# Kernel tuning notes

Hardware: AMD Instinct MI355X
Metric: run time of the kernel (lower is better)

## Reference

```python
import jax, jax.numpy as jnp
import numpy as np

RES = 64

TRI_TABLE = jnp.array([
    [-1,-1,-1,-1,-1,-1],[1,0,2,-1,-1,-1],[4,0,3,-1,-1,-1],[1,4,2,1,3,4],
    [3,1,5,-1,-1,-1],[2,3,0,2,5,3],[1,4,0,1,5,4],[4,2,5,-1,-1,-1],
    [4,5,2,-1,-1,-1],[4,1,0,4,5,1],[3,2,0,3,5,2],[1,3,5,-1,-1,-1],
    [4,1,2,4,3,1],[3,0,4,-1,-1,-1],[2,0,1,-1,-1,-1],[-1,-1,-1,-1,-1,-1]], dtype=jnp.int32)
NUM_TRI = jnp.array([0,1,1,2,1,2,2,1,1,2,2,1,2,1,1,0], dtype=jnp.int32)
BASE_EDGES = jnp.array([0,1,0,2,0,3,1,2,1,3,2,3], dtype=jnp.int32)


def _make_tet_grid(res):
    # Kuhn 6-tet decomposition of each cube of a (res+1)^3 grid.
    n = res + 1
    ii, jj, kk = np.meshgrid(np.arange(n), np.arange(n), np.arange(n), indexing='ij')
    verts = (np.stack([ii, jj, kk], -1).reshape(-1, 3).astype(np.float32)) / res
    def vid(i, j, k):
        return (i * n + j) * n + k
    i, j, k = np.meshgrid(np.arange(res), np.arange(res), np.arange(res), indexing='ij')
    i, j, k = i.ravel(), j.ravel(), k.ravel()
    c = [vid(i + (b & 1), j + ((b >> 1) & 1), k + ((b >> 2) & 1)) for b in range(8)]
    kuhn = [(0,1,3,7),(0,3,2,7),(0,2,6,7),(0,6,4,7),(0,4,5,7),(0,5,1,7)]
    tets = np.stack([np.stack([c[a], c[b], c[d], c[e]], -1) for (a, b, d, e) in kuhn], 1)
    return verts, tets.reshape(-1, 4).astype(np.int64)


def setup_inputs() -> dict:
    key = jax.random.key(0)
    verts, tets = _make_tet_grid(RES)
    level = jax.random.normal(key, (verts.shape[0], 1), dtype=jnp.float32)
    return {"level": level, "pos": jnp.asarray(verts), "tet": jnp.asarray(tets), "threshold": 0}


def reference(level, pos, tet, threshold):
    sdf = level - threshold                    # [N,1]
    occ = sdf[:, 0] > 0                        # [N]
    occ_fx4 = occ[tet]                         # [F,4]
    occ_sum = occ_fx4.sum(-1)
    valid = (occ_sum > 0) & (occ_sum < 4)
    vt = tet[valid]                            # [Fv,4]
    occ_valid = occ_fx4[valid]                 # [Fv,4]

    edges = jnp.sort(vt[:, BASE_EDGES].reshape(-1, 2), axis=1)   # [Fv*6,2]
    unique_edges, idx_map = jnp.unique(edges, axis=0, return_inverse=True)
    idx_map = idx_map.reshape(-1)
    mask_edges = occ[unique_edges].sum(-1) == 1                  # crossing edges
    mapping = jnp.where(mask_edges, jnp.cumsum(mask_edges) - 1, -1)
    idx_map = mapping[idx_map].reshape(-1, 6)                    # [Fv,6]
    interp_v = unique_edges[mask_edges]                          # [M,2]

    p = pos[interp_v]                                            # [M,2,3]
    s = sdf[interp_v][..., 0] * jnp.array([1.0, -1.0], dtype=sdf.dtype)  # [M,2]
    w = s[:, ::-1] / s.sum(1, keepdims=True)                     # flip / denom
    verts_out = (p * w[..., None]).sum(1)                        # [M,3]

    v_id = 2 ** jnp.arange(4, dtype=jnp.int32)
    tetindex = (occ_valid.astype(jnp.int32) * v_id).sum(-1)      # [Fv]
    num_tri = NUM_TRI[tetindex]
    m1, m2 = num_tri == 1, num_tri == 2
    f1 = jnp.take_along_axis(idx_map[m1], TRI_TABLE[tetindex[m1]][:, :3], axis=1).reshape(-1, 3)
    f2 = jnp.take_along_axis(idx_map[m2], TRI_TABLE[tetindex[m2]][:, :6], axis=1).reshape(-1, 3)
    faces = jnp.concatenate([f1, f2], axis=0)
    return verts_out, faces
```

## Files before the change

kernel.cpp:

```cpp
#include <hip/hip_runtime.h>


#define RESX 64
#define NV   65
#define NV2  4225
#define NVERT 274625
#define NCUBE 262144
#define BLOCK 256
#define NG64 4292
#define CG64 4096
#define NBLK1 1073
#define CBLK 1024
#define FOLD 49
#define WINW 80
#define STAGE 9216
#define M21 0x1fffffu
#define NTRI_PACK 0x16696994u

__constant__ int c_tri[16][6] = {
    {-1,-1,-1,-1,-1,-1},{1,0,2,-1,-1,-1},{4,0,3,-1,-1,-1},{1,4,2,1,3,4},
    {3,1,5,-1,-1,-1},{2,3,0,2,5,3},{1,4,0,1,5,4},{4,2,5,-1,-1,-1},
    {4,5,2,-1,-1,-1},{4,1,0,4,5,1},{3,2,0,3,5,2},{1,3,5,-1,-1,-1},
    {4,1,2,4,3,1},{3,0,4,-1,-1,-1},{2,0,1,-1,-1,-1},{-1,-1,-1,-1,-1,-1}};
__constant__ int c_kuhn[6][4] = {{0,1,3,7},{0,3,2,7},{0,2,6,7},{0,6,4,7},{0,4,5,7},{0,5,1,7}};
__constant__ int c_off8[8] = {0,4225,65,4290,1,4226,66,4291};
__constant__ int c_loc[6][6] = {
    {0,0,0,1,1,3},{0,0,0,2,3,2},{0,0,0,2,2,6},
    {0,0,0,4,6,4},{0,0,0,4,4,5},{0,0,0,1,5,1}};
__constant__ int c_dir[6][6] = {
    {3,5,6,1,2,0},{5,1,6,3,0,4},{1,2,6,0,4,3},
    {2,0,6,1,3,5},{0,4,6,3,5,1},{4,3,6,0,1,2}};

typedef unsigned long long u64;

__device__ __forceinline__ unsigned block_scan_excl(unsigned val, unsigned* lds,
                                                    unsigned& block_total) {
    int tid = threadIdx.x, lane = tid & 63, w = tid >> 6;
    unsigned x = val;
#pragma unroll
    for (int off = 1; off < 64; off <<= 1) {
        unsigned y = (unsigned)__shfl_up((int)x, off, 64);
        if (lane >= off) x += y;
    }
    if (lane == 63) lds[w] = x;
    __syncthreads();
    if (tid == 0) {
        unsigned s = 0;
#pragma unroll
        for (int i = 0; i < 4; i++) { unsigned t = lds[i]; lds[i + 4] = s; s += t; }
        lds[8] = s;
    }
    __syncthreads();
    block_total = lds[8];
    return x - val + lds[4 + w];
}

__global__ void __launch_bounds__(256)
pass1(const float* __restrict__ level, const float* __restrict__ thrp,
      unsigned char* __restrict__ flagsArr, unsigned short* __restrict__ locEx,
      u64* __restrict__ bsAll) {
    int tid = threadIdx.x, lane = tid & 63, w = tid >> 6;
    int g = blockIdx.x * 4 + w;
    float thr = thrp[0];
    int v = g * 64 + lane;

    unsigned fl = 0;
    if (g <= 4222) {
        float a0 = level[v]        - thr;
        float a1 = level[v + 1]    - thr;
        float a2 = level[v + 65]   - thr;
        float a3 = level[v + 66]   - thr;
        float a4 = level[v + 4225] - thr;
        float a5 = level[v + 4226] - thr;
        float a6 = level[v + 4290] - thr;
        float a7 = level[v + 4291] - thr;
        int i = v / NV2; int r = v - i * NV2; int j = r / NV; int k = r - j * NV;
        bool okx = i < RESX, oky = j < RESX, okz = k < RESX;
        bool s0 = a0 > 0.f;
        fl = s0 ? 0x80u : 0u;
        if (okz               && ((a1 > 0.f) != s0)) fl |= 1u;
        if (oky               && ((a2 > 0.f) != s0)) fl |= 2u;
        if (oky && okz        && ((a3 > 0.f) != s0)) fl |= 4u;
        if (okx               && ((a4 > 0.f) != s0)) fl |= 8u;
        if (okx && okz        && ((a5 > 0.f) != s0)) fl |= 16u;
        if (okx && oky        && ((a6 > 0.f) != s0)) fl |= 32u;
        if (okx && oky && okz && ((a7 > 0.f) != s0)) fl |= 64u;
    } else if (v < NVERT) {
        int i = v / NV2; int r = v - i * NV2; int j = r / NV; int k = r - j * NV;
        bool okx = i < RESX, oky = j < RESX, okz = k < RESX;
        float a0 = level[v] - thr;
        bool s0 = a0 > 0.f;
        fl = s0 ? 0x80u : 0u;
        if (okz               && (((level[v + 1]    - thr) > 0.f) != s0)) fl |= 1u;
        if (oky               && (((level[v + 65]   - thr) > 0.f) != s0)) fl |= 2u;
        if (oky && okz        && (((level[v + 66]   - thr) > 0.f) != s0)) fl |= 4u;
        if (okx               && (((level[v + 4225] - thr) > 0.f) != s0)) fl |= 8u;
        if (okx && okz        && (((level[v + 4226] - thr) > 0.f) != s0)) fl |= 16u;
        if (okx && oky        && (((level[v + 4290] - thr) > 0.f) != s0)) fl |= 32u;
        if (okx && oky && okz && (((level[v + 4291] - thr) > 0.f) != s0)) fl |= 64u;
    }
    unsigned cnt = __popc(fl & 0x7fu);
    unsigned x = cnt;
#pragma unroll
    for (int off = 1; off < 64; off <<= 1) {
        unsigned y = (unsigned)__shfl_up((int)x, off, 64);
        if (lane >= off) x += y;
    }
    unsigned wex = x - cnt;
    unsigned totE = (unsigned)__shfl((int)x, 63, 64);
    if (v < NVERT) {
        flagsArr[v] = (unsigned char)fl;
        locEx[v] = (unsigned short)wex;
    }

    unsigned c1 = 0, c2 = 0;
    if (g < CG64) {
        int c = g * 64 + lane;
        int ci = c >> 12, cj = (c >> 6) & 63, ck = c & 63;
        int base = (ci * NV + cj) * NV + ck;
        float q0 = level[base]        - thr;
        float q4 = level[base + 1]    - thr;
        float q2 = level[base + 65]   - thr;
        float q6 = level[base + 66]   - thr;
        float q1 = level[base + 4225] - thr;
        float q5 = level[base + 4226] - thr;
        float q3 = level[base + 4290] - thr;
        float q7 = level[base + 4291] - thr;
        unsigned occ8 = (q0 > 0.f ?   1u : 0u) | (q1 > 0.f ?   2u : 0u)
                      | (q2 > 0.f ?   4u : 0u) | (q3 > 0.f ?   8u : 0u)
                      | (q4 > 0.f ?  16u : 0u) | (q5 > 0.f ?  32u : 0u)
                      | (q6 > 0.f ?  64u : 0u) | (q7 > 0.f ? 128u : 0u);
#pragma unroll
        for (int t = 0; t < 6; t++) {
            int cfg = ((occ8 >> c_kuhn[t][0]) & 1) | (((occ8 >> c_kuhn[t][1]) & 1) << 1)
                    | (((occ8 >> c_kuhn[t][2]) & 1) << 2) | (((occ8 >> c_kuhn[t][3]) & 1) << 3);
            unsigned nt = (NTRI_PACK >> (cfg << 1)) & 3u;
            c1 += (nt == 1);
            c2 += (nt == 2);
        }
        unsigned pk = c1 | (c2 << 16);
#pragma unroll
        for (int off = 32; off; off >>= 1) pk += (unsigned)__shfl_xor((int)pk, off, 64);
        c1 = pk & 0xffffu; c2 = pk >> 16;
    }
    if (lane == 0)
        bsAll[g] = (u64)totE | ((u64)c1 << 16) | ((u64)c2 << 32);
}

__global__ void __launch_bounds__(1024)
scanK(const u64* __restrict__ bsAll, uint4* __restrict__ pre) {
    __shared__ u64 lws[16];
    int tid = threadIdx.x, lane = tid & 63, w = tid >> 6;
    int b0 = tid * 5;
    u64 vl[5]; u64 s = 0;
#pragma unroll
    for (int e = 0; e < 5; e++) {
        int idx = b0 + e;
        u64 a = (idx < NG64) ? bsAll[idx] : 0ull;
        u64 p = (a & 0xffffull) | (((a >> 16) & 0xffffull) << 21)
              | (((a >> 32) & 0xffffull) << 42);
        vl[e] = p; s += p;
    }
    u64 x = s;
#pragma unroll
    for (int off = 1; off < 64; off <<= 1) {
        u64 y = __shfl_up(x, off, 64);
        if (lane >= off) x += y;
    }
    if (lane == 63) lws[w] = x;
    __syncthreads();
    if (tid == 0) {
        u64 acc = 0;
#pragma unroll
        for (int i = 0; i < 16; i++) { u64 t = lws[i]; lws[i] = acc; acc += t; }
    }
    __syncthreads();
    u64 run = x - s + lws[w];
#pragma unroll
    for (int e = 0; e < 5; e++) {
        int idx = b0 + e;
        if (idx <= NG64)
            pre[idx] = make_uint4((unsigned)(run & M21), (unsigned)((run >> 21) & M21),
                                  (unsigned)(run >> 42), 0u);
        run += vl[e];
    }
}

__device__ __forceinline__ void emit_verts_stage(
        int gidv, unsigned slotBase, const float* __restrict__ level, float thr,
        const unsigned char* __restrict__ flagsArr,
        const unsigned short* __restrict__ locEx, float* stage) {
    float lv[8];
    int gsafe = (gidv < NVERT) ? gidv : 0;
#pragma unroll
    for (int b = 0; b < 8; b++) {
        int a = gsafe + c_off8[b];
        lv[b] = level[a < NVERT ? a : 0] - thr;
    }
    if (gidv < NVERT) {
        unsigned fl = flagsArr[gidv];
        if (fl & 0x7fu) {
            int i = gidv / NV2; int r = gidv - i * NV2; int j = r / NV; int k = r - j * NV;
            float v0 = lv[0];
            unsigned slot = slotBase + locEx[gidv];
            const float inv = 1.f / 64.f;
            const int d2b[7] = {4, 2, 6, 1, 5, 3, 7};
            float fi = (float)i, fj = (float)j, fk = (float)k;
#pragma unroll
            for (int d = 0; d < 7; d++) {
                if (fl & (1u << d)) {
                    const int b = d2b[d];
                    float s1 = lv[b];
                    float w1 = v0 * __builtin_amdgcn_rcpf(v0 - s1);
                    float* o = &stage[3u * slot];
                    o[0] = (fi + (float)(b & 1) * w1) * inv;
                    o[1] = (fj + (float)((b >> 1) & 1) * w1) * inv;
                    o[2] = (fk + (float)((b >> 2) & 1) * w1) * inv;
                    slot++;
                }
            }
        }
    }
}

__global__ void __launch_bounds__(256)
pass2(const float* __restrict__ level, const float* __restrict__ thrp,
      const unsigned char* __restrict__ flagsArr,
      const unsigned short* __restrict__ locEx,
      const uint4* __restrict__ pre, float* __restrict__ out) {
    __shared__ unsigned lds[9];
    __shared__ unsigned pEw[WINW];
    __shared__ float stage[STAGE];
    int tid = threadIdx.x;
    int bid = blockIdx.x;
    int gid = bid * BLOCK + tid;
    float thr = thrp[0];
    bool hasB = (bid < FOLD);

    uint4 pA = pre[4 * bid];
    uint4 pN = pre[4 * bid + 4];
    uint4 pt = pre[NG64];
    unsigned pE = pA.x, totE_blk = pN.x - pA.x;
    unsigned p1b = pA.y, p2b = pA.z;
    unsigned M = pt.x, C1 = pt.y;

    int ci = bid >> 4, cj0 = (bid & 15) * 4;
    int vmin = (ci * NV + cj0) * NV;
    int wb = vmin >> 6;
    if (tid < WINW) {
        int t = wb + tid;
        pEw[tid] = (t <= NG64) ? pre[t].x : M;
    }

    unsigned slotBase = pre[gid >> 6].x - pE;
    emit_verts_stage(gid, slotBase, level, thr, flagsArr, locEx, stage);
    __syncthreads();
    {
        float* dst = out + 3u * pE;
        unsigned n = totE_blk * 3u;
        for (unsigned idx = tid; idx < n; idx += BLOCK)
            __builtin_nontemporal_store(stage[idx], &dst[idx]);
    }
    if (hasB) {
        int gb0 = CG64 + 4 * bid;
        unsigned pEB = pre[gb0].x;
        unsigned totB = pre[gb0 + 4].x - pEB;
        int gidB = NCUBE + bid * BLOCK + tid;
        __syncthreads();
        unsigned sbB = pre[gidB >> 6].x - pEB;
        emit_verts_stage(gidB, sbB, level, thr, flagsArr, locEx, stage);
        __syncthreads();
        float* dst = out + 3u * pEB;
        unsigned n = totB * 3u;
        for (unsigned idx = tid; idx < n; idx += BLOCK)
            __builtin_nontemporal_store(stage[idx], &dst[idx]);
    }
    __syncthreads();

    int cci = gid >> 12, ccj = (gid >> 6) & 63, cck = gid & 63;
    int base = (cci * NV + ccj) * NV + cck;
    u64 f8 = 0ull;
#pragma unroll
    for (int b = 0; b < 8; b++)
        f8 |= (u64)flagsArr[base + c_off8[b]] << (8 * b);
    unsigned occ8 = 0;
#pragma unroll
    for (int b = 0; b < 8; b++) occ8 |= (unsigned)((f8 >> (8 * b + 7)) & 1ull) << b;
    int cfgs[6];
    unsigned c1 = 0, c2 = 0;
#pragma unroll
    for (int t = 0; t < 6; t++) {
        int cfg = ((occ8 >> c_kuhn[t][0]) & 1) | (((occ8 >> c_kuhn[t][1]) & 1) << 1)
                | (((occ8 >> c_kuhn[t][2]) & 1) << 2) | (((occ8 >> c_kuhn[t][3]) & 1) << 3);
        cfgs[t] = cfg;
        unsigned nt = (NTRI_PACK >> (cfg << 1)) & 3u;
        c1 += (nt == 1); c2 += (nt == 2);
    }
    unsigned tot2;
    unsigned ex2 = block_scan_excl(c1 | (c2 << 16), lds, tot2);
    unsigned f1 = tot2 & 0xffffu;
    unsigned f2 = tot2 >> 16;
    unsigned l1c = ex2 & 0xffffu;
    unsigned l2c = ex2 >> 16;
    unsigned n1 = f1 * 3u;
#pragma unroll
    for (int t = 0; t < 6; t++) {
        int cfg = cfgs[t];
        unsigned nt = (NTRI_PACK >> (cfg << 1)) & 3u;
        if (nt == 0) continue;
        auto rank = [&](int e) -> float {
            int lc = c_loc[t][e];
            int dir = c_dir[t][e];
            int lo = base + c_off8[lc];
            unsigned flb = (unsigned)((f8 >> (8 * lc)) & 0xffull);
            return (float)(pEw[(lo >> 6) - wb] + locEx[lo]
                           + __popc(flb & ((1u << dir) - 1u)));
        };
        float ra = rank(c_tri[cfg][0]);
        float rb = rank(c_tri[cfg][1]);
        float rc = rank(c_tri[cfg][2]);
        if (nt == 1) {
            unsigned bfo = 3u * l1c;
            stage[bfo] = ra; stage[bfo + 1] = rb; stage[bfo + 2] = rc;
            l1c++;
        } else {
            float rd = rank(c_tri[cfg][4]);
            unsigned bfo = n1 + 6u * l2c;
            stage[bfo]     = ra; stage[bfo + 1] = rb; stage[bfo + 2] = rc;
            stage[bfo + 3] = ra; stage[bfo + 4] = rd; stage[bfo + 5] = rb;
            l2c++;
        }
    }
    __syncthreads();
    float* of = out + 3ull * M;
    float* o1 = of + 3u * p1b;
    for (unsigned idx = tid; idx < n1; idx += BLOCK)
        __builtin_nontemporal_store(stage[idx], &o1[idx]);
    unsigned n2 = f2 * 6u;
    float* o2 = of + 3u * (C1 + 2u * p2b);
    for (unsigned idx = tid; idx < n2; idx += BLOCK)
        __builtin_nontemporal_store(stage[n1 + idx], &o2[idx]);
}

extern "C" void kernel_launch(void* const* d_in, const int* in_sizes, int n_in,
                              void* d_out, int out_size, void* d_ws, size_t ws_size,
                              hipStream_t stream) {
    const float* level = (const float*)d_in[0];
    const float* thrp = (const float*)d_in[3];
    float* out = (float*)d_out;

    char* p = (char*)d_ws;
    unsigned char* flagsArr = (unsigned char*)p;
    p += (NVERT + 255) & ~255;
    unsigned short* locEx = (unsigned short*)p;
    p += ((sizeof(unsigned short) * NVERT) + 255) & ~255;
    u64* bsAll = (u64*)p;
    p += ((sizeof(u64) * NG64) + 255) & ~255;
    uint4* pre = (uint4*)p;

    pass1<<<NBLK1, BLOCK, 0, stream>>>(level, thrp, flagsArr, locEx, bsAll);
    scanK<<<1, 1024, 0, stream>>>(bsAll, pre);
    pass2<<<CBLK, BLOCK, 0, stream>>>(level, thrp, flagsArr, locEx, pre, out);
}
```

Baseline: 110.6 us.

## Reorganize vertex grouping to grid rows with shuffle-based neighbor reuse

```diff
diff --git a/kernel.cpp b/kernel.cpp
--- a/kernel.cpp
+++ b/kernel.cpp
@@ -7,12 +7,13 @@
 #define NVERT 274625
 #define NCUBE 262144
 #define BLOCK 256
-#define NG64 4292
-#define CG64 4096
-#define NBLK1 1073
+#define NGE 4225
+#define NGC 4096
+#define NB1I 1024
+#define NBND 129
+#define NBLK1 1057
 #define CBLK 1024
-#define FOLD 49
-#define WINW 80
+#define NFB 33
 #define STAGE 9216
 #define M21 0x1fffffu
 #define NTRI_PACK 0x16696994u
@@ -58,202 +59,267 @@
 __global__ void __launch_bounds__(256)
 pass1(const float* __restrict__ level, const float* __restrict__ thrp,
       unsigned char* __restrict__ flagsArr, unsigned short* __restrict__ locEx,
-      u64* __restrict__ bsAll) {
+      unsigned* __restrict__ bsE, unsigned* __restrict__ bsC) {
     int tid = threadIdx.x, lane = tid & 63, w = tid >> 6;
-    int g = blockIdx.x * 4 + w;
+    int bid = blockIdx.x;
     float thr = thrp[0];
-    int v = g * 64 + lane;
-
-    unsigned fl = 0;
-    if (g <= 4222) {
-        float a0 = level[v]        - thr;
-        float a1 = level[v + 1]    - thr;
-        float a2 = level[v + 65]   - thr;
-        float a3 = level[v + 66]   - thr;
-        float a4 = level[v + 4225] - thr;
-        float a5 = level[v + 4226] - thr;
-        float a6 = level[v + 4290] - thr;
-        float a7 = level[v + 4291] - thr;
-        int i = v / NV2; int r = v - i * NV2; int j = r / NV; int k = r - j * NV;
-        bool okx = i < RESX, oky = j < RESX, okz = k < RESX;
-        bool s0 = a0 > 0.f;
+    unsigned fl = 0, fl65 = 0, c1 = 0, c2 = 0;
+    int base, grp, cgrp = -1;
+
+    if (bid < NB1I) {
+        int ci = bid >> 4, cj = ((bid & 15) << 2) + w;
+        grp = ci * NV + cj;
+        base = grp * NV;
+        int v = base + lane;
+        float r0  = level[v]        - thr;
+        float rY  = level[v + 65]   - thr;
+        float rX  = level[v + 4225] - thr;
+        float rXY = level[v + 4290] - thr;
+        float t0 = 0.f, tY = 0.f, tX = 0.f, tXY = 0.f;
+        if (lane == 63) {
+            t0  = level[base + 64]   - thr;
+            tY  = level[base + 129]  - thr;
+            tX  = level[base + 4289] - thr;
+            tXY = level[base + 4354] - thr;
+        }
+        float a4 = __shfl_down(r0, 1, 64);  if (lane == 63) a4 = t0;
+        float a6 = __shfl_down(rY, 1, 64);  if (lane == 63) a6 = tY;
+        float a5 = __shfl_down(rX, 1, 64);  if (lane == 63) a5 = tX;
+        float a7 = __shfl_down(rXY, 1, 64); if (lane == 63) a7 = tXY;
+        bool s0 = r0 > 0.f;
         fl = s0 ? 0x80u : 0u;
-        if (okz               && ((a1 > 0.f) != s0)) fl |= 1u;
-        if (oky               && ((a2 > 0.f) != s0)) fl |= 2u;
-        if (oky && okz        && ((a3 > 0.f) != s0)) fl |= 4u;
-        if (okx               && ((a4 > 0.f) != s0)) fl |= 8u;
-        if (okx && okz        && ((a5 > 0.f) != s0)) fl |= 16u;
-        if (okx && oky        && ((a6 > 0.f) != s0)) fl |= 32u;
-        if (okx && oky && okz && ((a7 > 0.f) != s0)) fl |= 64u;
-    } else if (v < NVERT) {
-        int i = v / NV2; int r = v - i * NV2; int j = r / NV; int k = r - j * NV;
-        bool okx = i < RESX, oky = j < RESX, okz = k < RESX;
-        float a0 = level[v] - thr;
-        bool s0 = a0 > 0.f;
-        fl = s0 ? 0x80u : 0u;
-        if (okz               && (((level[v + 1]    - thr) > 0.f) != s0)) fl |= 1u;
-        if (oky               && (((level[v + 65]   - thr) > 0.f) != s0)) fl |= 2u;
-        if (oky && okz        && (((level[v + 66]   - thr) > 0.f) != s0)) fl |= 4u;
-        if (okx               && (((level[v + 4225] - thr) > 0.f) != s0)) fl |= 8u;
-        if (okx && okz        && (((level[v + 4226] - thr) > 0.f) != s0)) fl |= 16u;
-        if (okx && oky        && (((level[v + 4290] - thr) > 0.f) != s0)) fl |= 32u;
-        if (okx && oky && okz && (((level[v + 4291] - thr) > 0.f) != s0)) fl |= 64u;
-    }
-    unsigned cnt = __popc(fl & 0x7fu);
-    unsigned x = cnt;
-#pragma unroll
-    for (int off = 1; off < 64; off <<= 1) {
-        unsigned y = (unsigned)__shfl_up((int)x, off, 64);
-        if (lane >= off) x += y;
-    }
-    unsigned wex = x - cnt;
-    unsigned totE = (unsigned)__shfl((int)x, 63, 64);
-    if (v < NVERT) {
-        flagsArr[v] = (unsigned char)fl;
-        locEx[v] = (unsigned short)wex;
-    }
-
-    unsigned c1 = 0, c2 = 0;
-    if (g < CG64) {
-        int c = g * 64 + lane;
-        int ci = c >> 12, cj = (c >> 6) & 63, ck = c & 63;
-        int base = (ci * NV + cj) * NV + ck;
-        float q0 = level[base]        - thr;
-        float q4 = level[base + 1]    - thr;
-        float q2 = level[base + 65]   - thr;
-        float q6 = level[base + 66]   - thr;
-        float q1 = level[base + 4225] - thr;
-        float q5 = level[base + 4226] - thr;
-        float q3 = level[base + 4290] - thr;
-        float q7 = level[base + 4291] - thr;
-        unsigned occ8 = (q0 > 0.f ?   1u : 0u) | (q1 > 0.f ?   2u : 0u)
-                      | (q2 > 0.f ?   4u : 0u) | (q3 > 0.f ?   8u : 0u)
-                      | (q4 > 0.f ?  16u : 0u) | (q5 > 0.f ?  32u : 0u)
-                      | (q6 > 0.f ?  64u : 0u) | (q7 > 0.f ? 128u : 0u);
+        if ((a4  > 0.f) != s0) fl |= 1u;
+        if ((rY  > 0.f) != s0) fl |= 2u;
+        if ((a6  > 0.f) != s0) fl |= 4u;
+        if ((rX  > 0.f) != s0) fl |= 8u;
+        if ((a5  > 0.f) != s0) fl |= 16u;
+        if ((rXY > 0.f) != s0) fl |= 32u;
+        if ((a7  > 0.f) != s0) fl |= 64u;
+        unsigned occ8 = (r0  > 0.f ?   1u : 0u) | (rX  > 0.f ?   2u : 0u)
+                      | (rY  > 0.f ?   4u : 0u) | (rXY > 0.f ?   8u : 0u)
+                      | (a4  > 0.f ?  16u : 0u) | (a5  > 0.f ?  32u : 0u)
+                      | (a6  > 0.f ?  64u : 0u) | (a7  > 0.f ? 128u : 0u);
 #pragma unroll
         for (int t = 0; t < 6; t++) {
             int cfg = ((occ8 >> c_kuhn[t][0]) & 1) | (((occ8 >> c_kuhn[t][1]) & 1) << 1)
                     | (((occ8 >> c_kuhn[t][2]) & 1) << 2) | (((occ8 >> c_kuhn[t][3]) & 1) << 3);
             unsigned nt = (NTRI_PACK >> (cfg << 1)) & 3u;
-            c1 += (nt == 1);
-            c2 += (nt == 2);
-        }
-        unsigned pk = c1 | (c2 << 16);
-#pragma unroll
-        for (int off = 32; off; off >>= 1) pk += (unsigned)__shfl_xor((int)pk, off, 64);
-        c1 = pk & 0xffffu; c2 = pk >> 16;
-    }
-    if (lane == 0)
-        bsAll[g] = (u64)totE | ((u64)c1 << 16) | ((u64)c2 << 32);
+            c1 += (nt == 1); c2 += (nt == 2);
+        }
+        if (lane == 63) {
+            bool s65 = t0 > 0.f;
+            fl65 = s65 ? 0x80u : 0u;
+            if ((tY  > 0.f) != s65) fl65 |= 2u;
+            if ((tX  > 0.f) != s65) fl65 |= 8u;
+            if ((tXY > 0.f) != s65) fl65 |= 32u;
+        }
+        cgrp = (ci << 6) + cj;
+    } else {
+        int bw = (bid - NB1I) * 4 + w;
+        if (bw >= NBND) return;
+        if (bw < 64) {
+            grp = bw * NV + 64;
+            base = grp * NV;
+            int v = base + lane;
+            float r0 = level[v]        - thr;
+            float rX = level[v + 4225] - thr;
+            float t0 = 0.f, tX = 0.f;
+            if (lane == 63) { t0 = level[base + 64] - thr; tX = level[base + 4289] - thr; }
+            float a1 = __shfl_down(r0, 1, 64); if (lane == 63) a1 = t0;
+            float a5 = __shfl_down(rX, 1, 64); if (lane == 63) a5 = tX;
+            bool s0 = r0 > 0.f;
+            fl = s0 ? 0x80u : 0u;
+            if ((a1 > 0.f) != s0) fl |= 1u;
+            if ((rX > 0.f) != s0) fl |= 8u;
+            if ((a5 > 0.f) != s0) fl |= 16u;
+            if (lane == 63) {
+                bool s65 = t0 > 0.f;
+                fl65 = s65 ? 0x80u : 0u;
+                if ((tX > 0.f) != s65) fl65 |= 8u;
+            }
+        } else if (bw < 128) {
+            int j = bw - 64;
+            grp = 64 * NV + j;
+            base = grp * NV;
+            int v = base + lane;
+            float r0 = level[v]      - thr;
+            float rY = level[v + 65] - thr;
+            float t0 = 0.f, tY = 0.f;
+            if (lane == 63) { t0 = level[base + 64] - thr; tY = level[base + 129] - thr; }
+            float a1 = __shfl_down(r0, 1, 64); if (lane == 63) a1 = t0;
+            float a3 = __shfl_down(rY, 1, 64); if (lane == 63) a3 = tY;
+            bool s0 = r0 > 0.f;
+            fl = s0 ? 0x80u : 0u;
+            if ((a1 > 0.f) != s0) fl |= 1u;
+            if ((rY > 0.f) != s0) fl |= 2u;
+            if ((a3 > 0.f) != s0) fl |= 4u;
+            if (lane == 63) {
+                bool s65 = t0 > 0.f;
+                fl65 = s65 ? 0x80u : 0u;
+                if ((tY > 0.f) != s65) fl65 |= 2u;
+            }
+        } else {
+            grp = 64 * NV + 64;
+            base = grp * NV;
+            int v = base + lane;
+            float r0 = level[v] - thr;
+            float t0 = 0.f;
+            if (lane == 63) t0 = level[base + 64] - thr;
+            float a1 = __shfl_down(r0, 1, 64); if (lane == 63) a1 = t0;
+            bool s0 = r0 > 0.f;
+            fl = s0 ? 0x80u : 0u;
+            if ((a1 > 0.f) != s0) fl |= 1u;
+            if (lane == 63) fl65 = (t0 > 0.f) ? 0x80u : 0u;
+        }
+    }
+
+    unsigned cnt65 = __popc(fl65 & 0x7fu);
+    unsigned cnt = __popc(fl & 0x7fu);
+    unsigned val = cnt | (c1 << 10) | (c2 << 20);
+    unsigned x = val;
+#pragma unroll
+    for (int off = 1; off < 64; off <<= 1) {
+        unsigned y = (unsigned)__shfl_up((int)x, off, 64);
+        if (lane >= off) x += y;
+    }
+    int v = base + lane;
+    flagsArr[v] = (unsigned char)fl;
+    locEx[v] = (unsigned short)((x - val) & 0x3ffu);
+    if (lane == 63) {
+        unsigned totE64 = x & 0x3ffu;
+        flagsArr[base + 64] = (unsigned char)fl65;
+        locEx[base + 64] = (unsigned short)totE64;
+        bsE[grp] = totE64 + cnt65;
+        if (cgrp >= 0)
+            bsC[cgrp] = ((x >> 10) & 0x3ffu) | (((x >> 20) & 0x3ffu) << 16);
+    }
 }
 
 __global__ void __launch_bounds__(1024)
-scanK(const u64* __restrict__ bsAll, uint4* __restrict__ pre) {
-    __shared__ u64 lws[16];
+scanK(const unsigned* __restrict__ bsE, const unsigned* __restrict__ bsC,
+      unsigned* __restrict__ preE, uint2* __restrict__ preC) {
+    __shared__ unsigned lws[16];
+    __shared__ u64 lwc[16];
     int tid = threadIdx.x, lane = tid & 63, w = tid >> 6;
-    int b0 = tid * 5;
-    u64 vl[5]; u64 s = 0;
+    unsigned ev[5]; unsigned s = 0;
 #pragma unroll
     for (int e = 0; e < 5; e++) {
-        int idx = b0 + e;
-        u64 a = (idx < NG64) ? bsAll[idx] : 0ull;
-        u64 p = (a & 0xffffull) | (((a >> 16) & 0xffffull) << 21)
-              | (((a >> 32) & 0xffffull) << 42);
-        vl[e] = p; s += p;
-    }
-    u64 x = s;
+        int idx = tid * 5 + e;
+        unsigned a = (idx < NGE) ? bsE[idx] : 0u;
+        ev[e] = a; s += a;
+    }
+    unsigned x = s;
 #pragma unroll
     for (int off = 1; off < 64; off <<= 1) {
-        u64 y = __shfl_up(x, off, 64);
+        unsigned y = (unsigned)__shfl_up((int)x, off, 64);
         if (lane >= off) x += y;
     }
     if (lane == 63) lws[w] = x;
+    __syncthreads();
+    if (tid == 0) {
+        unsigned acc = 0;
+#pragma unroll
+        for (int i = 0; i < 16; i++) { unsigned t = lws[i]; lws[i] = acc; acc += t; }
+    }
+    __syncthreads();
+    unsigned run = x - s + lws[w];
+#pragma unroll
+    for (int e = 0; e < 5; e++) {
+        int idx = tid * 5 + e;
+        if (idx <= NGE) preE[idx] = run;
+        run += ev[e];
+    }
+    u64 cv[4]; u64 cs = 0;
+#pragma unroll
+    for (int e = 0; e < 4; e++) {
+        int idx = tid * 4 + e;
+        unsigned a = (idx < NGC) ? bsC[idx] : 0u;
+        u64 p = (u64)(a & 0xffffu) | ((u64)(a >> 16) << 21);
+        cv[e] = p; cs += p;
+    }
+    u64 cx = cs;
+#pragma unroll
+    for (int off = 1; off < 64; off <<= 1) {
+        u64 y = __shfl_up(cx, off, 64);
+        if (lane >= off) cx += y;
+    }
+    if (lane == 63) lwc[w] = cx;
     __syncthreads();
     if (tid == 0) {
         u64 acc = 0;
 #pragma unroll
-        for (int i = 0; i < 16; i++) { u64 t = lws[i]; lws[i] = acc; acc += t; }
-    }
-    __syncthreads();
-    u64 run = x - s + lws[w];
-#pragma unroll
-    for (int e = 0; e < 5; e++) {
-        int idx = b0 + e;
-        if (idx <= NG64)
-            pre[idx] = make_uint4((unsigned)(run & M21), (unsigned)((run >> 21) & M21),
-                                  (unsigned)(run >> 42), 0u);
-        run += vl[e];
-    }
-}
-
-__device__ __forceinline__ void emit_verts_stage(
-        int gidv, unsigned slotBase, const float* __restrict__ level, float thr,
-        const unsigned char* __restrict__ flagsArr,
-        const unsigned short* __restrict__ locEx, float* stage) {
-    float lv[8];
-    int gsafe = (gidv < NVERT) ? gidv : 0;
-#pragma unroll
-    for (int b = 0; b < 8; b++) {
-        int a = gsafe + c_off8[b];
-        lv[b] = level[a < NVERT ? a : 0] - thr;
-    }
-    if (gidv < NVERT) {
-        unsigned fl = flagsArr[gidv];
-        if (fl & 0x7fu) {
-            int i = gidv / NV2; int r = gidv - i * NV2; int j = r / NV; int k = r - j * NV;
-            float v0 = lv[0];
-            unsigned slot = slotBase + locEx[gidv];
-            const float inv = 1.f / 64.f;
-            const int d2b[7] = {4, 2, 6, 1, 5, 3, 7};
-            float fi = (float)i, fj = (float)j, fk = (float)k;
-#pragma unroll
-            for (int d = 0; d < 7; d++) {
-                if (fl & (1u << d)) {
-                    const int b = d2b[d];
-                    float s1 = lv[b];
-                    float w1 = v0 * __builtin_amdgcn_rcpf(v0 - s1);
-                    float* o = &stage[3u * slot];
-                    o[0] = (fi + (float)(b & 1) * w1) * inv;
-                    o[1] = (fj + (float)((b >> 1) & 1) * w1) * inv;
-                    o[2] = (fk + (float)((b >> 2) & 1) * w1) * inv;
-                    slot++;
-                }
-            }
-        }
-    }
+        for (int i = 0; i < 16; i++) { u64 t = lwc[i]; lwc[i] = acc; acc += t; }
+    }
+    __syncthreads();
+    u64 crun = cx - cs + lwc[w];
+#pragma unroll
+    for (int e = 0; e < 4; e++) {
+        int idx = tid * 4 + e;
+        if (idx < NGC)
+            preC[idx] = make_uint2((unsigned)(crun & M21), (unsigned)((crun >> 21) & M21));
+        crun += cv[e];
+    }
+    if (tid == 1023)
+        preC[NGC] = make_uint2((unsigned)(crun & M21), (unsigned)((crun >> 21) & M21));
 }
 
 __global__ void __launch_bounds__(256)
 pass2(const float* __restrict__ level, const float* __restrict__ thrp,
       const unsigned char* __restrict__ flagsArr,
       const unsigned short* __restrict__ locEx,
-      const uint4* __restrict__ pre, float* __restrict__ out) {
+      const unsigned* __restrict__ preE, const uint2* __restrict__ preC,
+      float* __restrict__ out) {
     __shared__ unsigned lds[9];
-    __shared__ unsigned pEw[WINW];
+    __shared__ unsigned pEw[10];
     __shared__ float stage[STAGE];
-    int tid = threadIdx.x;
-    int bid = blockIdx.x;
+    int tid = threadIdx.x, bid = blockIdx.x;
     int gid = bid * BLOCK + tid;
     float thr = thrp[0];
-    bool hasB = (bid < FOLD);
-
-    uint4 pA = pre[4 * bid];
-    uint4 pN = pre[4 * bid + 4];
-    uint4 pt = pre[NG64];
-    unsigned pE = pA.x, totE_blk = pN.x - pA.x;
-    unsigned p1b = pA.y, p2b = pA.z;
-    unsigned M = pt.x, C1 = pt.y;
-
-    int ci = bid >> 4, cj0 = (bid & 15) * 4;
-    int vmin = (ci * NV + cj0) * NV;
-    int wb = vmin >> 6;
-    if (tid < WINW) {
-        int t = wb + tid;
-        pEw[tid] = (t <= NG64) ? pre[t].x : M;
-    }
-
-    unsigned slotBase = pre[gid >> 6].x - pE;
-    emit_verts_stage(gid, slotBase, level, thr, flagsArr, locEx, stage);
+    int ci = bid >> 4, cj0 = (bid & 15) << 2;
+    int grpA = ci * NV + cj0;
+    unsigned pE = preE[grpA];
+    unsigned totE_blk = preE[grpA + 4] - pE;
+    if (tid < 10) pEw[tid] = preE[(ci + tid / 5) * NV + cj0 + tid % 5];
+    uint2 pc = preC[4 * bid];
+    unsigned M = preE[NGE];
+    unsigned C1 = preC[NGC].x;
+
+    {
+        int u = tid;
+#pragma unroll
+        for (int pass = 0; pass < 2; pass++) {
+            if (pass == 1) { if (tid >= 4) break; u = 256 + tid; }
+            int jr = (u >= 195) ? 3 : (u >= 130) ? 2 : (u >= 65) ? 1 : 0;
+            int k = u - jr * 65;
+            int vid = (grpA + jr) * NV + k;
+            float lv[8];
+#pragma unroll
+            for (int b = 0; b < 8; b++) {
+                int a = vid + c_off8[b];
+                lv[b] = level[a < NVERT ? a : 0] - thr;
+            }
+            unsigned fl = flagsArr[vid];
+            if (fl & 0x7fu) {
+                unsigned slot = (preE[grpA + jr] - pE) + locEx[vid];
+                float v0 = lv[0];
+                const float inv = 1.f / 64.f;
+                const int d2b[7] = {4, 2, 6, 1, 5, 3, 7};
+                float fi = (float)ci, fj = (float)(cj0 + jr), fk = (float)k;
+                float* o = &stage[3u * slot];
+#pragma unroll
+                for (int d = 0; d < 7; d++) {
+                    if (fl & (1u << d)) {
+                        const int b = d2b[d];
+                        float w1 = v0 * __builtin_amdgcn_rcpf(v0 - lv[b]);
+                        o[0] = (fi + (float)(b & 1) * w1) * inv;
+                        o[1] = (fj + (float)((b >> 1) & 1) * w1) * inv;
+                        o[2] = (fk + (float)((b >> 2) & 1) * w1) * inv;
+                        o += 3;
+                    }
+                }
+            }
+        }
+    }
     __syncthreads();
     {
         float* dst = out + 3u * pE;
@@ -261,28 +327,70 @@
         for (unsigned idx = tid; idx < n; idx += BLOCK)
             __builtin_nontemporal_store(stage[idx], &dst[idx]);
     }
-    if (hasB) {
-        int gb0 = CG64 + 4 * bid;
-        unsigned pEB = pre[gb0].x;
-        unsigned totB = pre[gb0 + 4].x - pEB;
-        int gidB = NCUBE + bid * BLOCK + tid;
+    if (bid < NFB) {
         __syncthreads();
-        unsigned sbB = pre[gidB >> 6].x - pEB;
-        emit_verts_stage(gidB, sbB, level, thr, flagsArr, locEx, stage);
+        int u = tid;
+#pragma unroll
+        for (int pass = 0; pass < 2; pass++) {
+            if (pass == 1) { if (tid >= 4) break; u = 256 + tid; }
+            int gsel = (u >= 195) ? 3 : (u >= 130) ? 2 : (u >= 65) ? 1 : 0;
+            int k = u - gsel * 65;
+            int bg = 4 * bid + gsel;
+            if (bg < NBND) {
+                int i, j;
+                if (bg < 64) { i = bg; j = 64; }
+                else         { i = 64; j = bg - 64; }
+                int vid = (i * NV + j) * NV + k;
+                float lv[8];
+#pragma unroll
+                for (int b = 0; b < 8; b++) {
+                    int a = vid + c_off8[b];
+                    lv[b] = level[a < NVERT ? a : 0] - thr;
+                }
+                unsigned fl = flagsArr[vid];
+                if (fl & 0x7fu) {
+                    unsigned slot = locEx[vid];
+                    float v0 = lv[0];
+                    const float inv = 1.f / 64.f;
+                    const int d2b[7] = {4, 2, 6, 1, 5, 3, 7};
+                    float fi = (float)i, fj = (float)j, fk = (float)k;
+                    float* o = &stage[1365u * (unsigned)gsel + 3u * slot];
+#pragma unroll
+                    for (int d = 0; d < 7; d++) {
+                        if (fl & (1u << d)) {
+                            const int b = d2b[d];
+                            float w1 = v0 * __builtin_amdgcn_rcpf(v0 - lv[b]);
+                            o[0] = (fi + (float)(b & 1) * w1) * inv;
+                            o[1] = (fj + (float)((b >> 1) & 1) * w1) * inv;
+                            o[2] = (fk + (float)((b >> 2) & 1) * w1) * inv;
+                            o += 3;
+                        }
+                    }
+                }
+            }
+        }
         __syncthreads();
-        float* dst = out + 3u * pEB;
-        unsigned n = totB * 3u;
-        for (unsigned idx = tid; idx < n; idx += BLOCK)
-            __builtin_nontemporal_store(stage[idx], &dst[idx]);
-    }
-    __syncthreads();
-
-    int cci = gid >> 12, ccj = (gid >> 6) & 63, cck = gid & 63;
-    int base = (cci * NV + ccj) * NV + cck;
+#pragma unroll
+        for (int gsel = 0; gsel < 4; gsel++) {
+            int bg = 4 * bid + gsel;
+            if (bg >= NBND) break;
+            int grp = (bg < 64) ? bg * NV + 64 : 64 * NV + (bg - 64);
+            unsigned pg = preE[grp];
+            unsigned n = (preE[grp + 1] - pg) * 3u;
+            float* dst = out + 3u * pg;
+            for (unsigned idx = tid; idx < n; idx += BLOCK)
+                __builtin_nontemporal_store(stage[1365u * (unsigned)gsel + idx], &dst[idx]);
+        }
+    }
+    __syncthreads();
+
+    int ccj = (gid >> 6) & 63, cck = gid & 63;
+    int cj_rel = ccj & 3;
+    int basev = (ci * NV + ccj) * NV + cck;
     u64 f8 = 0ull;
 #pragma unroll
     for (int b = 0; b < 8; b++)
-        f8 |= (u64)flagsArr[base + c_off8[b]] << (8 * b);
+        f8 |= (u64)flagsArr[basev + c_off8[b]] << (8 * b);
     unsigned occ8 = 0;
 #pragma unroll
     for (int b = 0; b < 8; b++) occ8 |= (unsigned)((f8 >> (8 * b + 7)) & 1ull) << b;
@@ -311,10 +419,10 @@
         auto rank = [&](int e) -> float {
             int lc = c_loc[t][e];
             int dir = c_dir[t][e];
-            int lo = base + c_off8[lc];
+            int lo = basev + c_off8[lc];
             unsigned flb = (unsigned)((f8 >> (8 * lc)) & 0xffull);
-            return (float)(pEw[(lo >> 6) - wb] + locEx[lo]
-                           + __popc(flb & ((1u << dir) - 1u)));
+            int widx = (lc & 1) * 5 + cj_rel + ((lc >> 1) & 1);
+            return (float)(pEw[widx] + locEx[lo] + __popc(flb & ((1u << dir) - 1u)));
         };
         float ra = rank(c_tri[cfg][0]);
         float rb = rank(c_tri[cfg][1]);
@@ -333,11 +441,11 @@
     }
     __syncthreads();
     float* of = out + 3ull * M;
-    float* o1 = of + 3u * p1b;
+    float* o1 = of + 3u * pc.x;
     for (unsigned idx = tid; idx < n1; idx += BLOCK)
         __builtin_nontemporal_store(stage[idx], &o1[idx]);
     unsigned n2 = f2 * 6u;
-    float* o2 = of + 3u * (C1 + 2u * p2b);
+    float* o2 = of + 3u * (C1 + 2u * pc.y);
     for (unsigned idx = tid; idx < n2; idx += BLOCK)
         __builtin_nontemporal_store(stage[n1 + idx], &o2[idx]);
 }
@@ -354,11 +462,15 @@
     p += (NVERT + 255) & ~255;
     unsigned short* locEx = (unsigned short*)p;
     p += ((sizeof(unsigned short) * NVERT) + 255) & ~255;
-    u64* bsAll = (u64*)p;
-    p += ((sizeof(u64) * NG64) + 255) & ~255;
-    uint4* pre = (uint4*)p;
-
-    pass1<<<NBLK1, BLOCK, 0, stream>>>(level, thrp, flagsArr, locEx, bsAll);
-    scanK<<<1, 1024, 0, stream>>>(bsAll, pre);
-    pass2<<<CBLK, BLOCK, 0, stream>>>(level, thrp, flagsArr, locEx, pre, out);
+    unsigned* bsE = (unsigned*)p;
+    p += ((sizeof(unsigned) * NGE) + 255) & ~255;
+    unsigned* bsC = (unsigned*)p;
+    p += ((sizeof(unsigned) * NGC) + 255) & ~255;
+    unsigned* preE = (unsigned*)p;
+    p += ((sizeof(unsigned) * (NGE + 1)) + 255) & ~255;
+    uint2* preC = (uint2*)p;
+
+    pass1<<<NBLK1, BLOCK, 0, stream>>>(level, thrp, flagsArr, locEx, bsE, bsC);
+    scanK<<<1, 1024, 0, stream>>>(bsE, bsC, preE, preC);
+    pass2<<<CBLK, BLOCK, 0, stream>>>(level, thrp, flagsArr, locEx, preE, preC, out);
 }
```

Measured after the change: 112.5 us. No clear change (+1.7%).
